# Performance work log

Hardware: AMD Instinct MI355X
Metric: run time of the kernel (lower is better)

Reference implementation:

```python
import jax, jax.numpy as jnp
import numpy as np

N = 100_000
E = 1_600_000
HID = 128
HEADS = 4
HD = HID // HEADS
EPS = 1e-5


def _ln(x, g, b):
    m = jnp.mean(x, axis=-1, keepdims=True)
    v = jnp.mean((x - m) ** 2, axis=-1, keepdims=True)
    return (x - m) * jax.lax.rsqrt(v + EPS) * g + b


def setup_inputs() -> dict:
    key = jax.random.key(0)
    ks = jax.random.split(key, 12)
    xav = lambda k, i, o: jax.random.uniform(k, (i, o), jnp.float32, -1.0, 1.0) * (0.1 * np.sqrt(6.0 / (i + o)))
    return {
        "h": jax.random.normal(ks[0], (N, HID), jnp.float32),
        "src": jax.random.randint(ks[1], (E,), 0, N, jnp.int32),
        "dst": jax.random.randint(ks[2], (E,), 0, N, jnp.int32),
        "Wq": xav(ks[3], HID, HID), "bq": jnp.zeros((HID,), jnp.float32),
        "Wk": xav(ks[4], HID, HID), "bk": jnp.zeros((HID,), jnp.float32),
        "Wv": xav(ks[5], HID, HID), "bv": jnp.zeros((HID,), jnp.float32),
        "Wo": xav(ks[6], HID, HID), "bo": jnp.zeros((HID,), jnp.float32),
        "W1": xav(ks[7], HID, 2 * HID), "b1": jnp.zeros((2 * HID,), jnp.float32),
        "W2": xav(ks[8], 2 * HID, HID), "b2": jnp.zeros((HID,), jnp.float32),
        "g1": jnp.ones((HID,), jnp.float32), "be1": jnp.zeros((HID,), jnp.float32),
        "g2": jnp.ones((HID,), jnp.float32), "be2": jnp.zeros((HID,), jnp.float32),
    }


def reference(h, src, dst, Wq, bq, Wk, bk, Wv, bv, Wo, bo, W1, b1, W2, b2, g1, be1, g2, be2):
    scale = HD ** -0.5
    h_norm = _ln(h, g1, be1)
    Q = (h_norm @ Wq + bq).reshape(N, HEADS, HD)
    K = (h_norm @ Wk + bk).reshape(N, HEADS, HD)
    V = (h_norm @ Wv + bv).reshape(N, HEADS, HD)

    # edge scores: q[dst] . k[src]  -> [E, HEADS]
    scores = jnp.sum(Q[dst] * K[src], axis=-1) * scale

    # edge softmax per destination node (segment softmax)
    smax = jax.ops.segment_max(scores, dst, num_segments=N)  # [N, HEADS]
    ex = jnp.exp(scores - smax[dst])
    denom = jax.ops.segment_sum(ex, dst, num_segments=N)
    alpha = ex / denom[dst]  # [E, HEADS]

    # weighted aggregation: sum over incoming edges of alpha * v[src]
    msgs = alpha[:, :, None] * V[src]  # [E, HEADS, HD]
    h_new = jax.ops.segment_sum(msgs, dst, num_segments=N).reshape(N, HID)

    h_attn = h_new @ Wo + bo
    h = h + h_attn  # dropout = identity (eval)
    h2 = _ln(h, g2, be2)
    ffn = jax.nn.relu(h2 @ W1 + b1) @ W2 + b2
    return h + ffn
```

## Files before the change

### kernel.cpp

```cpp
#include <hip/hip_runtime.h>
#include <math.h>

#define HIDN 128
#define EPS 1e-5f
#define ATT_SCALE 0.17677669529663687f

typedef unsigned int  u32;
typedef unsigned short u16;
typedef __attribute__((ext_vector_type(8))) short bf16x8;
typedef __attribute__((ext_vector_type(4))) float f32x4;

__device__ __forceinline__ u16 f2b(float x) {
    u32 u = __float_as_uint(x);
    u += 0x7FFFu + ((u >> 16) & 1u);
    return (u16)(u >> 16);
}
__device__ __forceinline__ float b2f(u16 x) { return __uint_as_float(((u32)x) << 16); }

#define MFMA(a, b, c) __builtin_amdgcn_mfma_f32_16x16x32_bf16((a), (b), (c), 0, 0, 0)

__global__ __launch_bounds__(256) void k_ln1(
    const float* __restrict__ h, const float* __restrict__ g, const float* __restrict__ b,
    u16* __restrict__ hn, int n)
{
    const int row = blockIdx.x * 4 + (threadIdx.x >> 6);
    const int lane = threadIdx.x & 63;
    if (row >= n) return;
    float2 v = *(const float2*)&h[(size_t)row * HIDN + lane * 2];
    float s = v.x + v.y, s2 = v.x * v.x + v.y * v.y;
    #pragma unroll
    for (int m = 1; m < 64; m <<= 1) { s += __shfl_xor(s, m); s2 += __shfl_xor(s2, m); }
    float mean = s * (1.f / 128.f);
    float var  = s2 * (1.f / 128.f) - mean * mean;
    float rs   = rsqrtf(var + EPS);
    float2 gv = *(const float2*)&g[lane * 2];
    float2 bv = *(const float2*)&b[lane * 2];
    u16 o0 = f2b((v.x - mean) * rs * gv.x + bv.x);
    u16 o1 = f2b((v.y - mean) * rs * gv.y + bv.y);
    *(u32*)&hn[(size_t)row * HIDN + lane * 2] = (u32)o0 | ((u32)o1 << 16);
}

__global__ __launch_bounds__(256) void k_pack_all(
    const float* __restrict__ Wq, const float* __restrict__ Wk, const float* __restrict__ Wv,
    const float* __restrict__ Wo, const float* __restrict__ W1, const float* __restrict__ W2,
    u16* __restrict__ out)
{
    int idx = blockIdx.x * 256 + threadIdx.x;
    const float* W; int K, N, base, local;
    if      (idx <  2048) { W = Wq; K = 128; N = 128; base = 0;     local = idx; }
    else if (idx <  4096) { W = Wk; K = 128; N = 128; base = 16384; local = idx - 2048; }
    else if (idx <  6144) { W = Wv; K = 128; N = 128; base = 32768; local = idx - 4096; }
    else if (idx <  8192) { W = Wo; K = 128; N = 128; base = 49152; local = idx - 6144; }
    else if (idx < 12288) { W = W1; K = 128; N = 256; base = 65536; local = idx - 8192; }
    else if (idx < 16384) { W = W2; K = 256; N = 128; base = 98304; local = idx - 12288; }
    else return;
    const int KC = K >> 5;
    const int l  = local & 63;
    const int tc = local >> 6;
    const int c  = tc % KC;
    const int t  = tc / KC;
    const int col = l & 15, hg = l >> 4;
    const int kbase = c * 32 + hg * 8;
    u16 v[8];
    #pragma unroll
    for (int j = 0; j < 8; ++j) v[j] = f2b(W[(size_t)(kbase + j) * N + t * 16 + col]);
    uint4 o;
    o.x = (u32)v[0] | ((u32)v[1] << 16);
    o.y = (u32)v[2] | ((u32)v[3] << 16);
    o.z = (u32)v[4] | ((u32)v[5] << 16);
    o.w = (u32)v[6] | ((u32)v[7] << 16);
    *(uint4*)&out[base + local * 8] = o;
}

__global__ __launch_bounds__(256) void k_qkv(
    const u16* __restrict__ hn,
    const u16* __restrict__ Bq, const u16* __restrict__ Bk, const u16* __restrict__ Bv,
    const float* __restrict__ bq, const float* __restrict__ bk, const float* __restrict__ bv,
    u16* __restrict__ Q, u16* __restrict__ K, u16* __restrict__ V, int M)
{
    const int slab = blockIdx.x * 4 + (threadIdx.x >> 6);
    const int l = threadIdx.x & 63;
    const int r0 = slab * 16;
    if (r0 >= M) return;
    const int col = l & 15, hg = l >> 4;
    const u16* ar = hn + (size_t)(r0 + col) * 128 + hg * 8;
    bf16x8 a0 = *(const bf16x8*)(ar);
    bf16x8 a1 = *(const bf16x8*)(ar + 32);
    bf16x8 a2 = *(const bf16x8*)(ar + 64);
    bf16x8 a3 = *(const bf16x8*)(ar + 96);
    const u16*  Bs[3] = {Bq, Bk, Bv};
    const float* bs[3] = {bq, bk, bv};
    u16*        Os[3] = {Q, K, V};
    #pragma unroll
    for (int w = 0; w < 3; ++w) {
        const u16* Bp = Bs[w];
        const float* bias = bs[w];
        u16* O = Os[w];
        #pragma unroll
        for (int t = 0; t < 8; ++t) {
            float bb = bias[t * 16 + col];
            f32x4 c = {bb, bb, bb, bb};
            const u16* bp = Bp + t * 2048 + l * 8;
            c = MFMA(a0, *(const bf16x8*)(bp),        c);
            c = MFMA(a1, *(const bf16x8*)(bp + 512),  c);
            c = MFMA(a2, *(const bf16x8*)(bp + 1024), c);
            c = MFMA(a3, *(const bf16x8*)(bp + 1536), c);
            #pragma unroll
            for (int r = 0; r < 4; ++r)
                O[(size_t)(r0 + hg * 4 + r) * 128 + t * 16 + col] = f2b(c[r]);
        }
    }
}

#define BSH 8
#define CHUNK 4096

__global__ __launch_bounds__(256) void k_bcount(
    const int* __restrict__ dst, int* __restrict__ bcnt, int e)
{
    __shared__ int hist[512];
    const int tid = threadIdx.x;
    hist[tid] = 0; hist[tid + 256] = 0;
    __syncthreads();
    const int i0 = blockIdx.x * CHUNK;
    #pragma unroll
    for (int t = 0; t < CHUNK / 256; ++t) {
        int i = i0 + t * 256 + tid;
        if (i < e) atomicAdd(&hist[dst[i] >> BSH], 1);
    }
    __syncthreads();
    for (int j = tid; j < 512; j += 256) {
        int c = hist[j];
        if (c) atomicAdd(&bcnt[j], c);
    }
}

__global__ __launch_bounds__(512) void k_bscan(
    const int* __restrict__ bcnt, int* __restrict__ bbase, int* __restrict__ bcur, int nbuck)
{
    __shared__ int ts[512];
    const int tid = threadIdx.x;
    int v = (tid < nbuck) ? bcnt[tid] : 0;
    ts[tid] = v;
    __syncthreads();
    for (int off = 1; off < 512; off <<= 1) {
        int x = (tid >= off) ? ts[tid - off] : 0;
        __syncthreads();
        ts[tid] += x;
        __syncthreads();
    }
    int ex = ts[tid] - v;
    if (tid <= nbuck) bbase[tid] = ex;
    if (tid < nbuck)  bcur[tid]  = ex;
}

__global__ __launch_bounds__(256) void k_bscatter(
    const int* __restrict__ src, const int* __restrict__ dst,
    int* __restrict__ bcur, int2* __restrict__ ebuf, int e)
{
    __shared__ int hist[512];
    __shared__ int lbase[512];
    __shared__ int lrun[512];
    const int tid = threadIdx.x;
    hist[tid] = 0; hist[tid + 256] = 0;
    __syncthreads();
    const int i0 = blockIdx.x * CHUNK;
    #pragma unroll
    for (int t = 0; t < CHUNK / 256; ++t) {
        int i = i0 + t * 256 + tid;
        if (i < e) atomicAdd(&hist[dst[i] >> BSH], 1);
    }
    __syncthreads();
    for (int j = tid; j < 512; j += 256) {
        int c = hist[j];
        lrun[j] = 0;
        if (c) lbase[j] = atomicAdd(&bcur[j], c);
    }
    __syncthreads();
    #pragma unroll
    for (int t = 0; t < CHUNK / 256; ++t) {
        int i = i0 + t * 256 + tid;
        if (i < e) {
            int d = dst[i];
            int b = d >> BSH;
            int r = atomicAdd(&lrun[b], 1);
            ebuf[lbase[b] + r] = make_int2(src[i], d);
        }
    }
}

__global__ __launch_bounds__(256) void k_bbuild(
    const int2* __restrict__ ebuf, const int* __restrict__ bbase,
    int* __restrict__ cnt, int* __restrict__ offs, int* __restrict__ csrc, int n)
{
    __shared__ int ncnt[256];
    __shared__ int ts[256];
    __shared__ int nrun[256];
    const int tid = threadIdx.x;
    const int b = blockIdx.x;
    const int node0 = b << BSH;
    const int nn = min(256, n - node0);
    const int s = bbase[b];
    const int epb = bbase[b + 1] - s;

    ncnt[tid] = 0;
    __syncthreads();
    for (int i = tid; i < epb; i += 256)
        atomicAdd(&ncnt[ebuf[s + i].y & 255], 1);
    __syncthreads();
    int v = ncnt[tid];
    ts[tid] = v;
    __syncthreads();
    for (int off = 1; off < 256; off <<= 1) {
        int x = (tid >= off) ? ts[tid - off] : 0;
        __syncthreads();
        ts[tid] += x;
        __syncthreads();
    }
    int ex = ts[tid] - v;
    if (tid < nn) { cnt[node0 + tid] = v; offs[node0 + tid] = s + ex; }
    nrun[tid] = 0;
    __syncthreads();
    ncnt[tid] = ex;
    __syncthreads();
    for (int i = tid; i < epb; i += 256) {
        int2 p = ebuf[s + i];
        int d = p.y & 255;
        int r = atomicAdd(&nrun[d], 1);
        csrc[s + ncnt[d] + r] = p.x;
    }
}

__global__ __launch_bounds__(256) void k_edge(
    const u16* __restrict__ Qb, const u16* __restrict__ Kb, const u16* __restrict__ Vb,
    const int* __restrict__ offs, const int* __restrict__ cnt, const int* __restrict__ csrc,
    u16* __restrict__ hnew, int n)
{
    const int wid  = threadIdx.x >> 6;
    const int lane = threadIdx.x & 63;
    const int node = blockIdx.x * 4 + wid;
    if (node >= n) return;
    const int start = offs[node];
    const int deg   = cnt[node];

    const u32 qu = *(const u32*)&Qb[(size_t)node * 128 + lane * 2];
    const float q0 = b2f((u16)(qu & 0xFFFF));
    const float q1 = b2f((u16)(qu >> 16));

    float denom = 0.f, o0 = 0.f, o1 = 0.f;

    for (int base = 0; base < deg; base += 64) {
        int m = deg - base; if (m > 64) m = 64;
        int myidx = 0;
        if (lane < m) myidx = csrc[start + base + lane];
        int j = 0;
        for (; j + 4 <= m; j += 4) {
            int s0 = __shfl(myidx, j + 0);
            int s1 = __shfl(myidx, j + 1);
            int s2 = __shfl(myidx, j + 2);
            int s3 = __shfl(myidx, j + 3);
            const u32 k0 = *(const u32*)&Kb[(size_t)s0 * 128 + lane * 2];
            const u32 k1 = *(const u32*)&Kb[(size_t)s1 * 128 + lane * 2];
            const u32 k2 = *(const u32*)&Kb[(size_t)s2 * 128 + lane * 2];
            const u32 k3 = *(const u32*)&Kb[(size_t)s3 * 128 + lane * 2];
            const u32 v0 = *(const u32*)&Vb[(size_t)s0 * 128 + lane * 2];
            const u32 v1 = *(const u32*)&Vb[(size_t)s1 * 128 + lane * 2];
            const u32 v2 = *(const u32*)&Vb[(size_t)s2 * 128 + lane * 2];
            const u32 v3 = *(const u32*)&Vb[(size_t)s3 * 128 + lane * 2];
            float p0 = q0 * b2f((u16)(k0 & 0xFFFF)) + q1 * b2f((u16)(k0 >> 16));
            float p1 = q0 * b2f((u16)(k1 & 0xFFFF)) + q1 * b2f((u16)(k1 >> 16));
            float p2 = q0 * b2f((u16)(k2 & 0xFFFF)) + q1 * b2f((u16)(k2 >> 16));
            float p3 = q0 * b2f((u16)(k3 & 0xFFFF)) + q1 * b2f((u16)(k3 >> 16));
            p0 += __shfl_xor(p0, 1); p1 += __shfl_xor(p1, 1); p2 += __shfl_xor(p2, 1); p3 += __shfl_xor(p3, 1);
            p0 += __shfl_xor(p0, 2); p1 += __shfl_xor(p1, 2); p2 += __shfl_xor(p2, 2); p3 += __shfl_xor(p3, 2);
            p0 += __shfl_xor(p0, 4); p1 += __shfl_xor(p1, 4); p2 += __shfl_xor(p2, 4); p3 += __shfl_xor(p3, 4);
            p0 += __shfl_xor(p0, 8); p1 += __shfl_xor(p1, 8); p2 += __shfl_xor(p2, 8); p3 += __shfl_xor(p3, 8);
            float w0 = __expf(p0 * ATT_SCALE);
            float w1 = __expf(p1 * ATT_SCALE);
            float w2 = __expf(p2 * ATT_SCALE);
            float w3 = __expf(p3 * ATT_SCALE);
            denom += (w0 + w1) + (w2 + w3);
            o0 = fmaf(w0, b2f((u16)(v0 & 0xFFFF)), o0); o1 = fmaf(w0, b2f((u16)(v0 >> 16)), o1);
            o0 = fmaf(w1, b2f((u16)(v1 & 0xFFFF)), o0); o1 = fmaf(w1, b2f((u16)(v1 >> 16)), o1);
            o0 = fmaf(w2, b2f((u16)(v2 & 0xFFFF)), o0); o1 = fmaf(w2, b2f((u16)(v2 >> 16)), o1);
            o0 = fmaf(w3, b2f((u16)(v3 & 0xFFFF)), o0); o1 = fmaf(w3, b2f((u16)(v3 >> 16)), o1);
        }
        for (; j < m; ++j) {
            int s = __shfl(myidx, j);
            const u32 kk = *(const u32*)&Kb[(size_t)s * 128 + lane * 2];
            const u32 vv = *(const u32*)&Vb[(size_t)s * 128 + lane * 2];
            float p = q0 * b2f((u16)(kk & 0xFFFF)) + q1 * b2f((u16)(kk >> 16));
            p += __shfl_xor(p, 1); p += __shfl_xor(p, 2); p += __shfl_xor(p, 4); p += __shfl_xor(p, 8);
            float w = __expf(p * ATT_SCALE);
            denom += w;
            o0 = fmaf(w, b2f((u16)(vv & 0xFFFF)), o0);
            o1 = fmaf(w, b2f((u16)(vv >> 16)), o1);
        }
    }
    float inv = (deg > 0) ? (1.f / denom) : 0.f;
    u16 r0_ = f2b(o0 * inv), r1_ = f2b(o1 * inv);
    *(u32*)&hnew[(size_t)node * 128 + lane * 2] = (u32)r0_ | ((u32)r1_ << 16);
}

__global__ __launch_bounds__(256) void k_attnout(
    const u16* __restrict__ hnew, const u16* __restrict__ Bo, const float* __restrict__ bo,
    const float* __restrict__ h, const float* __restrict__ g2, const float* __restrict__ be2,
    float* __restrict__ h1, u16* __restrict__ h2, int M)
{
    const int slab = blockIdx.x * 4 + (threadIdx.x >> 6);
    const int l = threadIdx.x & 63;
    const int r0 = slab * 16;
    if (r0 >= M) return;
    const int col = l & 15, hg = l >> 4;
    const u16* ar = hnew + (size_t)(r0 + col) * 128 + hg * 8;
    bf16x8 a0 = *(const bf16x8*)(ar);
    bf16x8 a1 = *(const bf16x8*)(ar + 32);
    bf16x8 a2 = *(const bf16x8*)(ar + 64);
    bf16x8 a3 = *(const bf16x8*)(ar + 96);
    f32x4 acc[8];
    #pragma unroll
    for (int t = 0; t < 8; ++t) {
        float bb = bo[t * 16 + col];
        f32x4 c = {bb, bb, bb, bb};
        const u16* bp = Bo + t * 2048 + l * 8;
        c = MFMA(a0, *(const bf16x8*)(bp),        c);
        c = MFMA(a1, *(const bf16x8*)(bp + 512),  c);
        c = MFMA(a2, *(const bf16x8*)(bp + 1024), c);
        c = MFMA(a3, *(const bf16x8*)(bp + 1536), c);
        acc[t] = c;
    }
    float s[4] = {0, 0, 0, 0}, s2[4] = {0, 0, 0, 0};
    #pragma unroll
    for (int t = 0; t < 8; ++t) {
        #pragma unroll
        for (int r = 0; r < 4; ++r) {
            float x = acc[t][r] + h[(size_t)(r0 + hg * 4 + r) * 128 + t * 16 + col];
            acc[t][r] = x;
            s[r] += x; s2[r] += x * x;
        }
    }
    float mean[4], rs[4];
    #pragma unroll
    for (int r = 0; r < 4; ++r) {
        float a = s[r], b = s2[r];
        a += __shfl_xor(a, 1); b += __shfl_xor(b, 1);
        a += __shfl_xor(a, 2); b += __shfl_xor(b, 2);
        a += __shfl_xor(a, 4); b += __shfl_xor(b, 4);
        a += __shfl_xor(a, 8); b += __shfl_xor(b, 8);
        mean[r] = a * (1.f / 128.f);
        float var = b * (1.f / 128.f) - mean[r] * mean[r];
        rs[r] = rsqrtf(var + EPS);
    }
    #pragma unroll
    for (int t = 0; t < 8; ++t) {
        float g  = g2[t * 16 + col];
        float be = be2[t * 16 + col];
        #pragma unroll
        for (int r = 0; r < 4; ++r) {
            size_t idx = (size_t)(r0 + hg * 4 + r) * 128 + t * 16 + col;
            float x = acc[t][r];
            h1[idx] = x;
            h2[idx] = f2b((x - mean[r]) * rs[r] * g + be);
        }
    }
}

__global__ __launch_bounds__(256) void k_ffn1(
    const u16* __restrict__ h2, const u16* __restrict__ B1, const float* __restrict__ b1,
    u16* __restrict__ tb, int M)
{
    const int slab = blockIdx.x * 4 + (threadIdx.x >> 6);
    const int l = threadIdx.x & 63;
    const int r0 = slab * 16;
    if (r0 >= M) return;
    const int col = l & 15, hg = l >> 4;
    const u16* ar = h2 + (size_t)(r0 + col) * 128 + hg * 8;
    bf16x8 a0 = *(const bf16x8*)(ar);
    bf16x8 a1 = *(const bf16x8*)(ar + 32);
    bf16x8 a2 = *(const bf16x8*)(ar + 64);
    bf16x8 a3 = *(const bf16x8*)(ar + 96);
    #pragma unroll
    for (int t = 0; t < 16; ++t) {
        float bb = b1[t * 16 + col];
        f32x4 c = {bb, bb, bb, bb};
        const u16* bp = B1 + t * 2048 + l * 8;
        c = MFMA(a0, *(const bf16x8*)(bp),        c);
        c = MFMA(a1, *(const bf16x8*)(bp + 512),  c);
        c = MFMA(a2, *(const bf16x8*)(bp + 1024), c);
        c = MFMA(a3, *(const bf16x8*)(bp + 1536), c);
        #pragma unroll
        for (int r = 0; r < 4; ++r)
            tb[(size_t)(r0 + hg * 4 + r) * 256 + t * 16 + col] = f2b(fmaxf(c[r], 0.f));
    }
}

__global__ __launch_bounds__(256) void k_ffn2(
    const u16* __restrict__ tb, const u16* __restrict__ B2, const float* __restrict__ b2,
    const float* __restrict__ h1, float* __restrict__ out, int M)
{
    const int slab = blockIdx.x * 4 + (threadIdx.x >> 6);
    const int l = threadIdx.x & 63;
    const int r0 = slab * 16;
    if (r0 >= M) return;
    const int col = l & 15, hg = l >> 4;
    const u16* ar = tb + (size_t)(r0 + col) * 256 + hg * 8;
    bf16x8 a[8];
    #pragma unroll
    for (int i = 0; i < 8; ++i) a[i] = *(const bf16x8*)(ar + i * 32);
    #pragma unroll
    for (int t = 0; t < 8; ++t) {
        float bb = b2[t * 16 + col];
        f32x4 c = {bb, bb, bb, bb};
        const u16* bp = B2 + t * 4096 + l * 8;
        #pragma unroll
        for (int kc = 0; kc < 8; ++kc)
            c = MFMA(a[kc], *(const bf16x8*)(bp + kc * 512), c);
        #pragma unroll
        for (int r = 0; r < 4; ++r) {
            size_t idx = (size_t)(r0 + hg * 4 + r) * 128 + t * 16 + col;
            out[idx] = c[r] + h1[idx];
        }
    }
}

extern "C" void kernel_launch(void* const* d_in, const int* in_sizes, int n_in,
                              void* d_out, int out_size, void* d_ws, size_t ws_size,
                              hipStream_t stream)
{
    const float* h   = (const float*)d_in[0];
    const int*   src = (const int*)  d_in[1];
    const int*   dst = (const int*)  d_in[2];
    const float* Wq  = (const float*)d_in[3];
    const float* bq  = (const float*)d_in[4];
    const float* Wk  = (const float*)d_in[5];
    const float* bk  = (const float*)d_in[6];
    const float* Wv  = (const float*)d_in[7];
    const float* bv  = (const float*)d_in[8];
    const float* Wo  = (const float*)d_in[9];
    const float* bo  = (const float*)d_in[10];
    const float* W1  = (const float*)d_in[11];
    const float* b1  = (const float*)d_in[12];
    const float* W2  = (const float*)d_in[13];
    const float* b2  = (const float*)d_in[14];
    const float* g1  = (const float*)d_in[15];
    const float* be1 = (const float*)d_in[16];
    const float* g2  = (const float*)d_in[17];
    const float* be2 = (const float*)d_in[18];

    const int n = in_sizes[0] / HIDN;
    const int e = in_sizes[1];
    float* out = (float*)d_out;

    const int nbuck = (n + 255) >> BSH;

    char* p = (char*)d_ws;
    int* csrc  = (int*)p;              p += (size_t)e * 4;
    int* cnt   = (int*)p;              p += (size_t)n * 4;
    int* offs  = (int*)p;              p += (size_t)n * 4;
    int* bcnt  = (int*)p;              p += 512 * 4;
    int* bbase = (int*)p;              p += 512 * 4;
    int* bcur  = (int*)p;              p += 512 * 4;
    u16* wpack = (u16*)p;              p += 131072 * 2;
    const size_t NB = (size_t)n * HIDN * 2;
    u16* hn   = (u16*)p;               p += NB;
    u16* Qb   = (u16*)p;               p += NB;
    u16* Kb   = (u16*)p;               p += NB;
    u16* Vb   = (u16*)p;               p += NB;
    u16* hnew = (u16*)p;               p += NB;
    float* h1 = (float*)p;             p += (size_t)n * HIDN * 4;
    u16* h2 = hn;
    u16* tb = Qb;
    int2* ebuf = (int2*)h1;

    u16* Wq_p = wpack;
    u16* Wk_p = wpack + 16384;
    u16* Wv_p = wpack + 32768;
    u16* Wo_p = wpack + 49152;
    u16* W1_p = wpack + 65536;
    u16* W2_p = wpack + 98304;

    const int nslab = (n + 15) / 16;
    const int gemm_blocks = (nslab + 3) / 4;
    const int echunks = (e + CHUNK - 1) / CHUNK;

    hipMemsetAsync(bcnt, 0, 512 * sizeof(int), stream);

    k_bcount  <<<echunks, 256, 0, stream>>>(dst, bcnt, e);
    k_bscan   <<<1, 512, 0, stream>>>(bcnt, bbase, bcur, nbuck);
    k_bscatter<<<echunks, 256, 0, stream>>>(src, dst, bcur, ebuf, e);
    k_bbuild  <<<nbuck, 256, 0, stream>>>(ebuf, bbase, cnt, offs, csrc, n);

    k_pack_all<<<64, 256, 0, stream>>>(Wq, Wk, Wv, Wo, W1, W2, wpack);
    k_ln1    <<<(n + 3) / 4, 256, 0, stream>>>(h, g1, be1, hn, n);

    k_qkv    <<<gemm_blocks, 256, 0, stream>>>(hn, Wq_p, Wk_p, Wv_p, bq, bk, bv, Qb, Kb, Vb, n);

    k_edge   <<<(n + 3) / 4, 256, 0, stream>>>(Qb, Kb, Vb, offs, cnt, csrc, hnew, n);

    k_attnout<<<gemm_blocks, 256, 0, stream>>>(hnew, Wo_p, bo, h, g2, be2, h1, h2, n);

    k_ffn1   <<<gemm_blocks, 256, 0, stream>>>(h2, W1_p, b1, tb, n);

    k_ffn2   <<<gemm_blocks, 256, 0, stream>>>(tb, W2_p, b2, h1, out, n);
}
```

Before: 459.6 us.

## Fuse LN1 into QKV GEMM and fuse attn-out, LN2, FFN into one tail kernel

LayerNorm1 is computed inside the QKV GEMM from fp32 h, so the bf16 normalized buffer is no longer written and re-read. The Wo projection, residual, LayerNorm2, FFN1 and FFN2 are merged into a single kernel that keeps h1, h2 and the hidden FFN activations in registers and LDS, avoiding global round-trips. GEMM outputs are staged through swizzled LDS so global stores are written as coalesced vectors. The cost is extra LDS traffic, barriers, and higher register pressure in the fused tail kernel, which may lower occupancy.

After: 485.4 us. +5.6%, slower.

```diff
diff --git a/kernel.cpp b/kernel.cpp
--- a/kernel.cpp
+++ b/kernel.cpp
@@ -19,25 +19,11 @@
 
 #define MFMA(a, b, c) __builtin_amdgcn_mfma_f32_16x16x32_bf16((a), (b), (c), 0, 0, 0)
 
-__global__ __launch_bounds__(256) void k_ln1(
-    const float* __restrict__ h, const float* __restrict__ g, const float* __restrict__ b,
-    u16* __restrict__ hn, int n)
-{
-    const int row = blockIdx.x * 4 + (threadIdx.x >> 6);
-    const int lane = threadIdx.x & 63;
-    if (row >= n) return;
-    float2 v = *(const float2*)&h[(size_t)row * HIDN + lane * 2];
-    float s = v.x + v.y, s2 = v.x * v.x + v.y * v.y;
-    #pragma unroll
-    for (int m = 1; m < 64; m <<= 1) { s += __shfl_xor(s, m); s2 += __shfl_xor(s2, m); }
-    float mean = s * (1.f / 128.f);
-    float var  = s2 * (1.f / 128.f) - mean * mean;
-    float rs   = rsqrtf(var + EPS);
-    float2 gv = *(const float2*)&g[lane * 2];
-    float2 bv = *(const float2*)&b[lane * 2];
-    u16 o0 = f2b((v.x - mean) * rs * gv.x + bv.x);
-    u16 o1 = f2b((v.y - mean) * rs * gv.y + bv.y);
-    *(u32*)&hn[(size_t)row * HIDN + lane * 2] = (u32)o0 | ((u32)o1 << 16);
+__device__ __forceinline__ int swz(int row, int kpos, int rowstride) {
+    return row * rowstride + ((((kpos >> 3) ^ (row & 7)) << 3) | (kpos & 7));
+}
+__device__ __forceinline__ int swzf(int row, int kpos) {
+    return row * 128 + ((((kpos >> 2) ^ (row & 7)) << 2) | (kpos & 3));
 }
 
 __global__ __launch_bounds__(256) void k_pack_all(
@@ -73,21 +59,56 @@
 }
 
 __global__ __launch_bounds__(256) void k_qkv(
-    const u16* __restrict__ hn,
+    const float* __restrict__ h, const float* __restrict__ g1, const float* __restrict__ be1,
     const u16* __restrict__ Bq, const u16* __restrict__ Bk, const u16* __restrict__ Bv,
     const float* __restrict__ bq, const float* __restrict__ bk, const float* __restrict__ bv,
     u16* __restrict__ Q, u16* __restrict__ K, u16* __restrict__ V, int M)
 {
-    const int slab = blockIdx.x * 4 + (threadIdx.x >> 6);
-    const int l = threadIdx.x & 63;
-    const int r0 = slab * 16;
-    if (r0 >= M) return;
+    __shared__ u16 smem[4][2048];
+    const int wid = threadIdx.x >> 6;
+    const int l   = threadIdx.x & 63;
+    int slab = blockIdx.x * 4 + wid;
+    const bool valid = (slab * 16) < M;
+    if (!valid) slab = 0;
+    const int r0  = slab * 16;
     const int col = l & 15, hg = l >> 4;
-    const u16* ar = hn + (size_t)(r0 + col) * 128 + hg * 8;
-    bf16x8 a0 = *(const bf16x8*)(ar);
-    bf16x8 a1 = *(const bf16x8*)(ar + 32);
-    bf16x8 a2 = *(const bf16x8*)(ar + 64);
-    bf16x8 a3 = *(const bf16x8*)(ar + 96);
+    u16* ws = smem[wid];
+
+    float av[4][8];
+    const float* hr = h + (size_t)(r0 + col) * 128 + hg * 8;
+    #pragma unroll
+    for (int c = 0; c < 4; ++c) {
+        float4 p0 = *(const float4*)&hr[c * 32];
+        float4 p1 = *(const float4*)&hr[c * 32 + 4];
+        av[c][0] = p0.x; av[c][1] = p0.y; av[c][2] = p0.z; av[c][3] = p0.w;
+        av[c][4] = p1.x; av[c][5] = p1.y; av[c][6] = p1.z; av[c][7] = p1.w;
+    }
+    float s = 0.f, q2 = 0.f;
+    #pragma unroll
+    for (int c = 0; c < 4; ++c)
+        #pragma unroll
+        for (int j = 0; j < 8; ++j) { float v = av[c][j]; s += v; q2 += v * v; }
+    s  += __shfl_xor(s, 16);  s  += __shfl_xor(s, 32);
+    q2 += __shfl_xor(q2, 16); q2 += __shfl_xor(q2, 32);
+    float mean = s * (1.f / 128.f);
+    float var  = q2 * (1.f / 128.f) - mean * mean;
+    float rs   = rsqrtf(var + EPS);
+
+    bf16x8 af[4];
+    #pragma unroll
+    for (int c = 0; c < 4; ++c) {
+        u32 w[4];
+        #pragma unroll
+        for (int jj = 0; jj < 4; ++jj) {
+            int k0 = c * 32 + hg * 8 + 2 * jj;
+            float v0 = (av[c][2 * jj]     - mean) * rs * g1[k0]     + be1[k0];
+            float v1 = (av[c][2 * jj + 1] - mean) * rs * g1[k0 + 1] + be1[k0 + 1];
+            w[jj] = (u32)f2b(v0) | ((u32)f2b(v1) << 16);
+        }
+        uint4 uu = make_uint4(w[0], w[1], w[2], w[3]);
+        af[c] = *(bf16x8*)&uu;
+    }
+
     const u16*  Bs[3] = {Bq, Bk, Bv};
     const float* bs[3] = {bq, bk, bv};
     u16*        Os[3] = {Q, K, V};
@@ -95,20 +116,31 @@
     for (int w = 0; w < 3; ++w) {
         const u16* Bp = Bs[w];
         const float* bias = bs[w];
-        u16* O = Os[w];
         #pragma unroll
         for (int t = 0; t < 8; ++t) {
             float bb = bias[t * 16 + col];
             f32x4 c = {bb, bb, bb, bb};
             const u16* bp = Bp + t * 2048 + l * 8;
-            c = MFMA(a0, *(const bf16x8*)(bp),        c);
-            c = MFMA(a1, *(const bf16x8*)(bp + 512),  c);
-            c = MFMA(a2, *(const bf16x8*)(bp + 1024), c);
-            c = MFMA(a3, *(const bf16x8*)(bp + 1536), c);
+            c = MFMA(af[0], *(const bf16x8*)(bp),        c);
+            c = MFMA(af[1], *(const bf16x8*)(bp + 512),  c);
+            c = MFMA(af[2], *(const bf16x8*)(bp + 1024), c);
+            c = MFMA(af[3], *(const bf16x8*)(bp + 1536), c);
             #pragma unroll
             for (int r = 0; r < 4; ++r)
-                O[(size_t)(r0 + hg * 4 + r) * 128 + t * 16 + col] = f2b(c[r]);
-        }
+                ws[swz(hg * 4 + r, t * 16 + col, 128)] = f2b(c[r]);
+        }
+        __syncthreads();
+        if (valid) {
+            u16* O = Os[w];
+            #pragma unroll
+            for (int i = 0; i < 4; ++i) {
+                int row = i * 4 + (l >> 4);
+                int cg  = l & 15;
+                bf16x8 vv = *(const bf16x8*)&ws[swz(row, cg * 8, 128)];
+                *(bf16x8*)&O[(size_t)(r0 + row) * 128 + cg * 8] = vv;
+            }
+        }
+        __syncthreads();
     }
 }
 
@@ -302,22 +334,30 @@
     *(u32*)&hnew[(size_t)node * 128 + lane * 2] = (u32)r0_ | ((u32)r1_ << 16);
 }
 
-__global__ __launch_bounds__(256) void k_attnout(
+__global__ __launch_bounds__(256) void k_tail(
     const u16* __restrict__ hnew, const u16* __restrict__ Bo, const float* __restrict__ bo,
     const float* __restrict__ h, const float* __restrict__ g2, const float* __restrict__ be2,
-    float* __restrict__ h1, u16* __restrict__ h2, int M)
-{
-    const int slab = blockIdx.x * 4 + (threadIdx.x >> 6);
-    const int l = threadIdx.x & 63;
-    const int r0 = slab * 16;
-    if (r0 >= M) return;
+    const u16* __restrict__ B1, const float* __restrict__ b1,
+    const u16* __restrict__ B2, const float* __restrict__ b2,
+    float* __restrict__ out, int M)
+{
+    __shared__ u16 smem[4][4096];
+    const int wid = threadIdx.x >> 6;
+    const int l   = threadIdx.x & 63;
+    int slab = blockIdx.x * 4 + wid;
+    const bool valid = (slab * 16) < M;
+    if (!valid) slab = 0;
+    const int r0  = slab * 16;
     const int col = l & 15, hg = l >> 4;
+    u16* ws = smem[wid];
+
     const u16* ar = hnew + (size_t)(r0 + col) * 128 + hg * 8;
     bf16x8 a0 = *(const bf16x8*)(ar);
     bf16x8 a1 = *(const bf16x8*)(ar + 32);
     bf16x8 a2 = *(const bf16x8*)(ar + 64);
     bf16x8 a3 = *(const bf16x8*)(ar + 96);
-    f32x4 acc[8];
+    float h1v[8][4];
+    float s[4] = {0, 0, 0, 0}, s2[4] = {0, 0, 0, 0};
     #pragma unroll
     for (int t = 0; t < 8; ++t) {
         float bb = bo[t * 16 + col];
@@ -327,15 +367,10 @@
         c = MFMA(a1, *(const bf16x8*)(bp + 512),  c);
         c = MFMA(a2, *(const bf16x8*)(bp + 1024), c);
         c = MFMA(a3, *(const bf16x8*)(bp + 1536), c);
-        acc[t] = c;
-    }
-    float s[4] = {0, 0, 0, 0}, s2[4] = {0, 0, 0, 0};
-    #pragma unroll
-    for (int t = 0; t < 8; ++t) {
         #pragma unroll
         for (int r = 0; r < 4; ++r) {
-            float x = acc[t][r] + h[(size_t)(r0 + hg * 4 + r) * 128 + t * 16 + col];
-            acc[t][r] = x;
+            float x = c[r] + h[(size_t)(r0 + hg * 4 + r) * 128 + t * 16 + col];
+            h1v[t][r] = x;
             s[r] += x; s2[r] += x * x;
         }
     }
@@ -356,57 +391,36 @@
         float g  = g2[t * 16 + col];
         float be = be2[t * 16 + col];
         #pragma unroll
-        for (int r = 0; r < 4; ++r) {
-            size_t idx = (size_t)(r0 + hg * 4 + r) * 128 + t * 16 + col;
-            float x = acc[t][r];
-            h1[idx] = x;
-            h2[idx] = f2b((x - mean[r]) * rs[r] * g + be);
-        }
-    }
-}
-
-__global__ __launch_bounds__(256) void k_ffn1(
-    const u16* __restrict__ h2, const u16* __restrict__ B1, const float* __restrict__ b1,
-    u16* __restrict__ tb, int M)
-{
-    const int slab = blockIdx.x * 4 + (threadIdx.x >> 6);
-    const int l = threadIdx.x & 63;
-    const int r0 = slab * 16;
-    if (r0 >= M) return;
-    const int col = l & 15, hg = l >> 4;
-    const u16* ar = h2 + (size_t)(r0 + col) * 128 + hg * 8;
-    bf16x8 a0 = *(const bf16x8*)(ar);
-    bf16x8 a1 = *(const bf16x8*)(ar + 32);
-    bf16x8 a2 = *(const bf16x8*)(ar + 64);
-    bf16x8 a3 = *(const bf16x8*)(ar + 96);
+        for (int r = 0; r < 4; ++r)
+            ws[swz(hg * 4 + r, t * 16 + col, 128)] =
+                f2b((h1v[t][r] - mean[r]) * rs[r] * g + be);
+    }
+    __syncthreads();
+    bf16x8 f1[4];
+    #pragma unroll
+    for (int i = 0; i < 4; ++i)
+        f1[i] = *(const bf16x8*)&ws[swz(col, i * 32 + hg * 8, 128)];
+    __syncthreads();
     #pragma unroll
     for (int t = 0; t < 16; ++t) {
         float bb = b1[t * 16 + col];
         f32x4 c = {bb, bb, bb, bb};
         const u16* bp = B1 + t * 2048 + l * 8;
-        c = MFMA(a0, *(const bf16x8*)(bp),        c);
-        c = MFMA(a1, *(const bf16x8*)(bp + 512),  c);
-        c = MFMA(a2, *(const bf16x8*)(bp + 1024), c);
-        c = MFMA(a3, *(const bf16x8*)(bp + 1536), c);
+        c = MFMA(f1[0], *(const bf16x8*)(bp),        c);
+        c = MFMA(f1[1], *(const bf16x8*)(bp + 512),  c);
+        c = MFMA(f1[2], *(const bf16x8*)(bp + 1024), c);
+        c = MFMA(f1[3], *(const bf16x8*)(bp + 1536), c);
         #pragma unroll
         for (int r = 0; r < 4; ++r)
-            tb[(size_t)(r0 + hg * 4 + r) * 256 + t * 16 + col] = f2b(fmaxf(c[r], 0.f));
-    }
-}
-
-__global__ __launch_bounds__(256) void k_ffn2(
-    const u16* __restrict__ tb, const u16* __restrict__ B2, const float* __restrict__ b2,
-    const float* __restrict__ h1, float* __restrict__ out, int M)
-{
-    const int slab = blockIdx.x * 4 + (threadIdx.x >> 6);
-    const int l = threadIdx.x & 63;
-    const int r0 = slab * 16;
-    if (r0 >= M) return;
-    const int col = l & 15, hg = l >> 4;
-    const u16* ar = tb + (size_t)(r0 + col) * 256 + hg * 8;
-    bf16x8 a[8];
-    #pragma unroll
-    for (int i = 0; i < 8; ++i) a[i] = *(const bf16x8*)(ar + i * 32);
+            ws[swz(hg * 4 + r, t * 16 + col, 256)] = f2b(fmaxf(c[r], 0.f));
+    }
+    __syncthreads();
+    bf16x8 f2[8];
+    #pragma unroll
+    for (int i = 0; i < 8; ++i)
+        f2[i] = *(const bf16x8*)&ws[swz(col, i * 32 + hg * 8, 256)];
+    __syncthreads();
+    float* wsf = (float*)ws;
     #pragma unroll
     for (int t = 0; t < 8; ++t) {
         float bb = b2[t * 16 + col];
@@ -414,11 +428,19 @@
         const u16* bp = B2 + t * 4096 + l * 8;
         #pragma unroll
         for (int kc = 0; kc < 8; ++kc)
-            c = MFMA(a[kc], *(const bf16x8*)(bp + kc * 512), c);
-        #pragma unroll
-        for (int r = 0; r < 4; ++r) {
-            size_t idx = (size_t)(r0 + hg * 4 + r) * 128 + t * 16 + col;
-            out[idx] = c[r] + h1[idx];
+            c = MFMA(f2[kc], *(const bf16x8*)(bp + kc * 512), c);
+        #pragma unroll
+        for (int r = 0; r < 4; ++r)
+            wsf[swzf(hg * 4 + r, t * 16 + col)] = c[r] + h1v[t][r];
+    }
+    __syncthreads();
+    if (valid) {
+        #pragma unroll
+        for (int i = 0; i < 8; ++i) {
+            int row = i * 2 + (l >> 5);
+            int cg  = l & 31;
+            float4 v = *(const float4*)&wsf[swzf(row, cg * 4)];
+            *(float4*)&out[(size_t)(r0 + row) * 128 + cg * 4] = v;
         }
     }
 }
@@ -462,15 +484,11 @@
     int* bcur  = (int*)p;              p += 512 * 4;
     u16* wpack = (u16*)p;              p += 131072 * 2;
     const size_t NB = (size_t)n * HIDN * 2;
-    u16* hn   = (u16*)p;               p += NB;
     u16* Qb   = (u16*)p;               p += NB;
     u16* Kb   = (u16*)p;               p += NB;
     u16* Vb   = (u16*)p;               p += NB;
     u16* hnew = (u16*)p;               p += NB;
-    float* h1 = (float*)p;             p += (size_t)n * HIDN * 4;
-    u16* h2 = hn;
-    u16* tb = Qb;
-    int2* ebuf = (int2*)h1;
+    int2* ebuf = (int2*)p;             p += (size_t)e * 8;
 
     u16* Wq_p = wpack;
     u16* Wk_p = wpack + 16384;
@@ -491,15 +509,12 @@
     k_bbuild  <<<nbuck, 256, 0, stream>>>(ebuf, bbase, cnt, offs, csrc, n);
 
     k_pack_all<<<64, 256, 0, stream>>>(Wq, Wk, Wv, Wo, W1, W2, wpack);
-    k_ln1    <<<(n + 3) / 4, 256, 0, stream>>>(h, g1, be1, hn, n);
-
-    k_qkv    <<<gemm_blocks, 256, 0, stream>>>(hn, Wq_p, Wk_p, Wv_p, bq, bk, bv, Qb, Kb, Vb, n);
-
-    k_edge   <<<(n + 3) / 4, 256, 0, stream>>>(Qb, Kb, Vb, offs, cnt, csrc, hnew, n);
-
-    k_attnout<<<gemm_blocks, 256, 0, stream>>>(hnew, Wo_p, bo, h, g2, be2, h1, h2, n);
-
-    k_ffn1   <<<gemm_blocks, 256, 0, stream>>>(h2, W1_p, b1, tb, n);
-
-    k_ffn2   <<<gemm_blocks, 256, 0, stream>>>(tb, W2_p, b2, h1, out, n);
-}
+
+    k_qkv <<<gemm_blocks, 256, 0, stream>>>(h, g1, be1, Wq_p, Wk_p, Wv_p,
+                                            bq, bk, bv, Qb, Kb, Vb, n);
+
+    k_edge<<<(n + 3) / 4, 256, 0, stream>>>(Qb, Kb, Vb, offs, cnt, csrc, hnew, n);
+
+    k_tail<<<gemm_blocks, 256, 0, stream>>>(hnew, Wo_p, bo, h, g2, be2,
+                                            W1_p, b1, W2_p, b2, out, n);
+}
```
